# Kernel optimization log

Hardware: AMD Instinct MI355X
Metric: run time of the kernel (lower is better)

Reference implementation:

```python
import jax, jax.numpy as jnp
import numpy as np

DT = 0.001
TAU_SYN_INV = 200.0
TAU_MEM_INV = 100.0
V_TH = 1.0

SEQ_LEN, BATCH, IN_DIM, HIDDEN, OUT_DIM = 1000, 128, 5, 512, 2


def setup_inputs() -> dict:
    key = jax.random.key(0)
    k_x, k_in, k_rec, k_out = jax.random.split(key, 4)
    x = jax.random.normal(k_x, (SEQ_LEN, BATCH, IN_DIM), dtype=jnp.float32)
    # input, recurrent and readout weights (Kaiming-ish scaling)
    w_in = jax.random.normal(k_in, (HIDDEN, IN_DIM), dtype=jnp.float32) / np.sqrt(IN_DIM)
    w_rec = jax.random.normal(k_rec, (HIDDEN, HIDDEN), dtype=jnp.float32) / np.sqrt(HIDDEN)
    w_out = jax.random.normal(k_out, (OUT_DIM, HIDDEN), dtype=jnp.float32) / np.sqrt(HIDDEN)
    return {"x": x, "w_in": w_in, "w_rec": w_rec, "w_out": w_out}


def _snn_forward(x, w_in, w_rec, w_out):
    T, B, _ = x.shape
    H, O = w_rec.shape[0], w_out.shape[0]
    dtype = x.dtype
    beta_syn = 1.0 - DT * TAU_SYN_INV  # synaptic current decay

    def step(carry, x_t):
        z, v, i, vo, io = carry
        # recurrent LIF layer
        i_in = x_t @ w_in.T + z @ w_rec.T            # [B,H]
        v_dec = v + DT * TAU_MEM_INV * (-v + i)      # leaky membrane integration
        z_new = (v_dec > V_TH).astype(dtype)         # spike (heaviside)
        v_new = jnp.where(z_new > 0, 0.0, v_dec)     # reset to v_reset=0
        i_new = i * beta_syn + i_in
        # linear readout (no bias) into LI feedforward cell
        y = z_new @ w_out.T                          # [B,O]
        vo_new = vo + DT * TAU_MEM_INV * (-vo + io)
        io_new = io * beta_syn + y
        return (z_new, v_new, i_new, vo_new, io_new), vo_new

    init = (
        jnp.zeros((B, H), dtype), jnp.zeros((B, H), dtype), jnp.zeros((B, H), dtype),
        jnp.zeros((B, O), dtype), jnp.zeros((B, O), dtype),
    )
    _, voltages = jax.lax.scan(step, init, x)
    return voltages  # [T, B, O] stacked readout voltages


def reference(x, w_in, w_rec, w_out):
    return _snn_forward(x, w_in, w_rec, w_out)
```

## Files before the change

### kernel.cpp

```cpp
#include <hip/hip_runtime.h>

#define HID 512
#define TSTEPS 1000
#define NB 128
#define NIN 5
#define NOUT 2

__global__ void snn_prep(const float* __restrict__ w_rec, float* __restrict__ wT) {
  int idx = blockIdx.x * 256 + threadIdx.x;
  if (idx < (HID + 1) * HID) {
    int j = idx >> 9;
    int h = idx & (HID - 1);
    wT[idx] = (j < HID) ? w_rec[h * HID + j] : 0.0f;
  }
}

__global__ __launch_bounds__(HID) void snn_main(
    const float* __restrict__ x,
    const float* __restrict__ w_in,
    const float* __restrict__ w_out,
    const float* __restrict__ wT,
    float* __restrict__ out)
{
#pragma clang fp contract(off)
  const int b = blockIdx.x;
  const int tid = threadIdx.x;
  const int lane = tid & 63;
  const int wv = tid >> 6;

  __shared__ unsigned long long s_mask[8];
  __shared__ int __align__(16) s_list[HID + 32];
  __shared__ float s_y[16];
  __shared__ float s_x[2][8];

  const float win0 = w_in[tid * NIN + 0];
  const float win1 = w_in[tid * NIN + 1];
  const float win2 = w_in[tid * NIN + 2];
  const float win3 = w_in[tid * NIN + 3];
  const float win4 = w_in[tid * NIN + 4];
  const float wo0 = w_out[tid];
  const float wo1 = w_out[HID + tid];

  float v = 0.0f, cur = 0.0f;
  float vo = 0.0f, io = 0.0f;

  if (tid < NIN) s_x[0][tid] = x[b * NIN + tid];
  __syncthreads();

  int total = 0;

  for (int t = 0; t < TSTEPS; ++t) {
    float racc = 0.0f;
    int n = 0;
    for (; n + 64 < total; n += 32) {
      int idxs[32];
#pragma unroll
      for (int q = 0; q < 8; ++q) {
        int4 jv = *reinterpret_cast<const int4*>(&s_list[n + 4 * q]);
        idxs[4 * q + 0] = jv.x; idxs[4 * q + 1] = jv.y;
        idxs[4 * q + 2] = jv.z; idxs[4 * q + 3] = jv.w;
      }
      float wbuf[32];
#pragma unroll
      for (int k = 0; k < 32; ++k) wbuf[k] = wT[idxs[k] * HID + tid];
#pragma unroll
      for (int k = 0; k < 32; ++k) racc = __fadd_rn(racc, wbuf[k]);
    }
    const bool hasA = (n < total);
    const bool hasB = (n + 32 < total);
    float wbufA[32], wbufB[32];
    if (hasA) {
      int idxs[32];
#pragma unroll
      for (int q = 0; q < 8; ++q) {
        int4 jv = *reinterpret_cast<const int4*>(&s_list[n + 4 * q]);
        idxs[4 * q + 0] = jv.x; idxs[4 * q + 1] = jv.y;
        idxs[4 * q + 2] = jv.z; idxs[4 * q + 3] = jv.w;
      }
#pragma unroll
      for (int k = 0; k < 32; ++k) wbufA[k] = wT[idxs[k] * HID + tid];
    }
    if (hasB) {
      int idxs[32];
#pragma unroll
      for (int q = 0; q < 8; ++q) {
        int4 jv = *reinterpret_cast<const int4*>(&s_list[n + 32 + 4 * q]);
        idxs[4 * q + 0] = jv.x; idxs[4 * q + 1] = jv.y;
        idxs[4 * q + 2] = jv.z; idxs[4 * q + 3] = jv.w;
      }
#pragma unroll
      for (int k = 0; k < 32; ++k) wbufB[k] = wT[idxs[k] * HID + tid];
    }

    const float* sx = s_x[t & 1];
    float a = __fmul_rn(sx[0], win0);
    a = fmaf(sx[1], win1, a);
    a = fmaf(sx[2], win2, a);
    a = fmaf(sx[3], win3, a);
    a = fmaf(sx[4], win4, a);

    const float vd = __fadd_rn(v, __fmul_rn(0.1f, __fsub_rn(cur, v)));
    const bool spike = vd > 1.0f;
    v = spike ? 0.0f : vd;

    float r0 = spike ? wo0 : 0.0f;
    float r1 = spike ? wo1 : 0.0f;
#pragma unroll
    for (int off = 1; off < 64; off <<= 1) {
      r0 = __fadd_rn(r0, __shfl_xor(r0, off, 64));
      r1 = __fadd_rn(r1, __shfl_xor(r1, off, 64));
    }
    const unsigned long long m = __ballot(spike);
    if (lane == 0) { s_mask[wv] = m; s_y[wv] = r0; s_y[8 + wv] = r1; }
    if (t + 1 < TSTEPS && tid < NIN)
      s_x[(t + 1) & 1][tid] = x[(size_t)(t + 1) * NB * NIN + b * NIN + tid];

    if (hasA) {
#pragma unroll
      for (int k = 0; k < 32; ++k) racc = __fadd_rn(racc, wbufA[k]);
    }
    if (hasB) {
#pragma unroll
      for (int k = 0; k < 32; ++k) racc = __fadd_rn(racc, wbufB[k]);
    }
    cur = __fadd_rn(__fmul_rn(0.8f, cur), __fadd_rn(a, racc));

    __syncthreads();

    int base = 0, tot = 0;
#pragma unroll
    for (int w2 = 0; w2 < 8; ++w2) {
      const int c = __popcll(s_mask[w2]);
      base += (w2 < wv) ? c : 0;
      tot += c;
    }
    if (spike) {
      const int pos = base + __popcll(m & ((1ull << lane) - 1ull));
      s_list[pos] = tid;
    }
    const int padded = (tot + 31) & ~31;
    if (tid >= tot && tid < padded) s_list[tid] = HID;

    if (tid < NOUT) {
      float y = 0.0f;
#pragma unroll
      for (int w2 = 0; w2 < 8; ++w2) y = __fadd_rn(y, s_y[tid * 8 + w2]);
      const float von = __fadd_rn(vo, __fmul_rn(0.1f, __fsub_rn(io, vo)));
      io = __fadd_rn(__fmul_rn(0.8f, io), y);
      vo = von;
      out[(size_t)t * NB * NOUT + b * NOUT + tid] = von;
    }

    __syncthreads();
    total = padded;
  }
}

extern "C" void kernel_launch(void* const* d_in, const int* in_sizes, int n_in,
                              void* d_out, int out_size, void* d_ws, size_t ws_size,
                              hipStream_t stream) {
  const float* x     = (const float*)d_in[0];
  const float* w_in  = (const float*)d_in[1];
  const float* w_rec = (const float*)d_in[2];
  const float* w_out = (const float*)d_in[3];
  float* out = (float*)d_out;
  float* wT = (float*)d_ws;

  const int prep_elems = (HID + 1) * HID;
  snn_prep<<<(prep_elems + 255) / 256, 256, 0, stream>>>(w_rec, wT);
  snn_main<<<NB, HID, 0, stream>>>(x, w_in, w_out, wT, out);
}
```

Measured before the change: 1.577 ms.

## Process two neurons per thread and fold readout into sparse spike gather

Each thread now handles two hidden neurons and loads float2 weight pairs from a padded transposed weight matrix. That matrix also carries the readout weights as extra columns, so the readout is computed by the same sparse gather as the recurrent input. Spike lists are built per wave into double-buffered segments with byte offsets and a packed count word, which removes one of the two block barriers per timestep. Output writes are deferred by one step, and x is prefetched into registers. In exchange the block holds fewer threads, each with more serial gather work, and the addressing becomes more complex.

```diff
diff --git a/kernel.cpp b/kernel.cpp
--- a/kernel.cpp
+++ b/kernel.cpp
@@ -5,21 +5,30 @@
 #define NB 128
 #define NIN 5
 #define NOUT 2
+#define ROWW 516
+#define ROWB (ROWW * 4)
+#define DUMMYOFF (HID * ROWB)
 
-__global__ void snn_prep(const float* __restrict__ w_rec, float* __restrict__ wT) {
+__global__ void snn_prep(const float* __restrict__ w_rec,
+                         const float* __restrict__ w_out,
+                         float* __restrict__ wT2) {
   int idx = blockIdx.x * 256 + threadIdx.x;
-  if (idx < (HID + 1) * HID) {
-    int j = idx >> 9;
-    int h = idx & (HID - 1);
-    wT[idx] = (j < HID) ? w_rec[h * HID + j] : 0.0f;
+  const int total = (HID + 1) * ROWW;
+  if (idx >= total) return;
+  int j = idx / ROWW;
+  int h = idx - j * ROWW;
+  float v = 0.0f;
+  if (j < HID) {
+    if (h < HID) v = w_rec[h * HID + j];
+    else if (h < HID + NOUT) v = w_out[(h - HID) * HID + j];
   }
+  wT2[idx] = v;
 }
 
-__global__ __launch_bounds__(HID) void snn_main(
+__global__ __launch_bounds__(320) void snn_main(
     const float* __restrict__ x,
     const float* __restrict__ w_in,
-    const float* __restrict__ w_out,
-    const float* __restrict__ wT,
+    const float* __restrict__ wT2,
     float* __restrict__ out)
 {
 #pragma clang fp contract(off)
@@ -27,132 +36,145 @@
   const int tid = threadIdx.x;
   const int lane = tid & 63;
   const int wv = tid >> 6;
+  const int h0 = tid * 2;
 
-  __shared__ unsigned long long s_mask[8];
-  __shared__ int __align__(16) s_list[HID + 32];
-  __shared__ float s_y[16];
-  __shared__ float s_x[2][8];
+  __shared__ int __align__(16) s_seg[2][4][132];
+  __shared__ unsigned int s_pcnt[2];
 
-  const float win0 = w_in[tid * NIN + 0];
-  const float win1 = w_in[tid * NIN + 1];
-  const float win2 = w_in[tid * NIN + 2];
-  const float win3 = w_in[tid * NIN + 3];
-  const float win4 = w_in[tid * NIN + 4];
-  const float wo0 = w_out[tid];
-  const float wo1 = w_out[HID + tid];
+  float wi00 = 0, wi01 = 0, wi02 = 0, wi03 = 0, wi04 = 0;
+  float wi10 = 0, wi11 = 0, wi12 = 0, wi13 = 0, wi14 = 0;
+  if (tid < 256) {
+    const float* wa = w_in + h0 * NIN;
+    wi00 = wa[0]; wi01 = wa[1]; wi02 = wa[2]; wi03 = wa[3]; wi04 = wa[4];
+    const float* wb = w_in + (h0 + 1) * NIN;
+    wi10 = wb[0]; wi11 = wb[1]; wi12 = wb[2]; wi13 = wb[3]; wi14 = wb[4];
+  }
 
-  float v = 0.0f, cur = 0.0f;
-  float vo = 0.0f, io = 0.0f;
+  float v0 = 0, v1 = 0, c0 = 0, c1 = 0;
+  float io0 = 0, io1 = 0, vo0 = 0, vo1 = 0;
+  float pend0 = 0, pend1 = 0;
 
-  if (tid < NIN) s_x[0][tid] = x[b * NIN + tid];
+  float xr0, xr1, xr2, xr3, xr4;
+  {
+    const float* xp = x + (size_t)b * NIN;
+    xr0 = xp[0]; xr1 = xp[1]; xr2 = xp[2]; xr3 = xp[3]; xr4 = xp[4];
+  }
+
+  if (tid == 0) s_pcnt[0] = 0;
   __syncthreads();
 
-  int total = 0;
+  const char* wtb = (const char*)wT2 + (size_t)h0 * 4;
 
   for (int t = 0; t < TSTEPS; ++t) {
-    float racc = 0.0f;
-    int n = 0;
-    for (; n + 64 < total; n += 32) {
-      int idxs[32];
-#pragma unroll
-      for (int q = 0; q < 8; ++q) {
-        int4 jv = *reinterpret_cast<const int4*>(&s_list[n + 4 * q]);
-        idxs[4 * q + 0] = jv.x; idxs[4 * q + 1] = jv.y;
-        idxs[4 * q + 2] = jv.z; idxs[4 * q + 3] = jv.w;
-      }
-      float wbuf[32];
-#pragma unroll
-      for (int k = 0; k < 32; ++k) wbuf[k] = wT[idxs[k] * HID + tid];
-#pragma unroll
-      for (int k = 0; k < 32; ++k) racc = __fadd_rn(racc, wbuf[k]);
-    }
-    const bool hasA = (n < total);
-    const bool hasB = (n + 32 < total);
-    float wbufA[32], wbufB[32];
-    if (hasA) {
-      int idxs[32];
-#pragma unroll
-      for (int q = 0; q < 8; ++q) {
-        int4 jv = *reinterpret_cast<const int4*>(&s_list[n + 4 * q]);
-        idxs[4 * q + 0] = jv.x; idxs[4 * q + 1] = jv.y;
-        idxs[4 * q + 2] = jv.z; idxs[4 * q + 3] = jv.w;
-      }
-#pragma unroll
-      for (int k = 0; k < 32; ++k) wbufA[k] = wT[idxs[k] * HID + tid];
-    }
-    if (hasB) {
-      int idxs[32];
-#pragma unroll
-      for (int q = 0; q < 8; ++q) {
-        int4 jv = *reinterpret_cast<const int4*>(&s_list[n + 32 + 4 * q]);
-        idxs[4 * q + 0] = jv.x; idxs[4 * q + 1] = jv.y;
-        idxs[4 * q + 2] = jv.z; idxs[4 * q + 3] = jv.w;
-      }
-#pragma unroll
-      for (int k = 0; k < 32; ++k) wbufB[k] = wT[idxs[k] * HID + tid];
+    const int rb = t & 1, wbuf = rb ^ 1;
+
+    if (tid == 256 && t > 0) {
+      float2 po; po.x = pend0; po.y = pend1;
+      *(float2*)(out + (size_t)(t - 1) * NB * NOUT + b * NOUT) = po;
     }
 
-    const float* sx = s_x[t & 1];
-    float a = __fmul_rn(sx[0], win0);
-    a = fmaf(sx[1], win1, a);
-    a = fmaf(sx[2], win2, a);
-    a = fmaf(sx[3], win3, a);
-    a = fmaf(sx[4], win4, a);
-
-    const float vd = __fadd_rn(v, __fmul_rn(0.1f, __fsub_rn(cur, v)));
-    const bool spike = vd > 1.0f;
-    v = spike ? 0.0f : vd;
-
-    float r0 = spike ? wo0 : 0.0f;
-    float r1 = spike ? wo1 : 0.0f;
-#pragma unroll
-    for (int off = 1; off < 64; off <<= 1) {
-      r0 = __fadd_rn(r0, __shfl_xor(r0, off, 64));
-      r1 = __fadd_rn(r1, __shfl_xor(r1, off, 64));
-    }
-    const unsigned long long m = __ballot(spike);
-    if (lane == 0) { s_mask[wv] = m; s_y[wv] = r0; s_y[8 + wv] = r1; }
-    if (t + 1 < TSTEPS && tid < NIN)
-      s_x[(t + 1) & 1][tid] = x[(size_t)(t + 1) * NB * NIN + b * NIN + tid];
-
-    if (hasA) {
-#pragma unroll
-      for (int k = 0; k < 32; ++k) racc = __fadd_rn(racc, wbufA[k]);
-    }
-    if (hasB) {
-#pragma unroll
-      for (int k = 0; k < 32; ++k) racc = __fadd_rn(racc, wbufB[k]);
-    }
-    cur = __fadd_rn(__fmul_rn(0.8f, cur), __fadd_rn(a, racc));
-
-    __syncthreads();
-
-    int base = 0, tot = 0;
-#pragma unroll
-    for (int w2 = 0; w2 < 8; ++w2) {
-      const int c = __popcll(s_mask[w2]);
-      base += (w2 < wv) ? c : 0;
-      tot += c;
-    }
-    if (spike) {
-      const int pos = base + __popcll(m & ((1ull << lane) - 1ull));
-      s_list[pos] = tid;
-    }
-    const int padded = (tot + 31) & ~31;
-    if (tid >= tot && tid < padded) s_list[tid] = HID;
-
-    if (tid < NOUT) {
-      float y = 0.0f;
-#pragma unroll
-      for (int w2 = 0; w2 < 8; ++w2) y = __fadd_rn(y, s_y[tid * 8 + w2]);
-      const float von = __fadd_rn(vo, __fmul_rn(0.1f, __fsub_rn(io, vo)));
-      io = __fadd_rn(__fmul_rn(0.8f, io), y);
-      vo = von;
-      out[(size_t)t * NB * NOUT + b * NOUT + tid] = von;
+    float nx0, nx1, nx2, nx3, nx4;
+    {
+      const int tn = (t + 1 < TSTEPS) ? t + 1 : t;
+      const float* xp = x + ((size_t)tn * NB + b) * NIN;
+      nx0 = xp[0]; nx1 = xp[1]; nx2 = xp[2]; nx3 = xp[3]; nx4 = xp[4];
     }
 
+    const unsigned int pw = s_pcnt[rb];
+    int pc0 = __builtin_amdgcn_readfirstlane((int)(pw & 255u));
+    int pc1 = __builtin_amdgcn_readfirstlane((int)((pw >> 8) & 255u));
+    int pc2 = __builtin_amdgcn_readfirstlane((int)((pw >> 16) & 255u));
+    int pc3 = __builtin_amdgcn_readfirstlane((int)((pw >> 24) & 255u));
+    const int b1 = pc0, b2v = b1 + pc1, b3v = b2v + pc2;
+    const int tot = b3v + pc3;
+    const int ng = tot >> 2;
+
+    float racc0 = 0.0f, racc1 = 0.0f;
+    if (h0 < HID + NOUT) {
+      const char* segbase = (const char*)&s_seg[rb][0][0];
+
+#define SEGADDR(GI, AP) { int w_ = 0, bw_ = 0;                         \
+      if ((GI) >= b1)  { w_ = 1; bw_ = b1;  }                          \
+      if ((GI) >= b2v) { w_ = 2; bw_ = b2v; }                          \
+      if ((GI) >= b3v) { w_ = 3; bw_ = b3v; }                          \
+      AP = segbase + w_ * 528 + ((GI) - bw_) * 4; }
+#define STAGE(JJ, F0, F1, F2, F3, G) { const char* ap_;                \
+      SEGADDR((G) * 4, ap_);                                           \
+      JJ = *(const int4*)ap_;                                          \
+      F0 = *(const float2*)(wtb + JJ.x);                               \
+      F1 = *(const float2*)(wtb + JJ.y);                               \
+      F2 = *(const float2*)(wtb + JJ.z);                               \
+      F3 = *(const float2*)(wtb + JJ.w); }
+#define CONSUME(F0, F1, F2, F3) {                                      \
+      racc0 = __fadd_rn(racc0, F0.x); racc1 = __fadd_rn(racc1, F0.y);  \
+      racc0 = __fadd_rn(racc0, F1.x); racc1 = __fadd_rn(racc1, F1.y);  \
+      racc0 = __fadd_rn(racc0, F2.x); racc1 = __fadd_rn(racc1, F2.y);  \
+      racc0 = __fadd_rn(racc0, F3.x); racc1 = __fadd_rn(racc1, F3.y); }
+
+      if (ng > 0) {
+        int4 jA, jB;
+        float2 a0, a1, a2, a3, q0, q1, q2, q3;
+        STAGE(jA, a0, a1, a2, a3, 0);
+        int g = 1;
+        for (; g + 1 < ng; g += 2) {
+          STAGE(jB, q0, q1, q2, q3, g);
+          CONSUME(a0, a1, a2, a3);
+          STAGE(jA, a0, a1, a2, a3, g + 1);
+          CONSUME(q0, q1, q2, q3);
+        }
+        if (g < ng) {
+          STAGE(jB, q0, q1, q2, q3, g);
+          CONSUME(a0, a1, a2, a3);
+          CONSUME(q0, q1, q2, q3);
+        } else {
+          CONSUME(a0, a1, a2, a3);
+        }
+      }
+    }
+
+    if (tid < 256) {
+      float a0 = __fmul_rn(xr0, wi00);
+      a0 = fmaf(xr1, wi01, a0); a0 = fmaf(xr2, wi02, a0);
+      a0 = fmaf(xr3, wi03, a0); a0 = fmaf(xr4, wi04, a0);
+      float a1 = __fmul_rn(xr0, wi10);
+      a1 = fmaf(xr1, wi11, a1); a1 = fmaf(xr2, wi12, a1);
+      a1 = fmaf(xr3, wi13, a1); a1 = fmaf(xr4, wi14, a1);
+
+      const float vd0 = __fadd_rn(v0, __fmul_rn(0.1f, __fsub_rn(c0, v0)));
+      const float vd1 = __fadd_rn(v1, __fmul_rn(0.1f, __fsub_rn(c1, v1)));
+      const bool s0 = vd0 > 1.0f;
+      const bool s1 = vd1 > 1.0f;
+      v0 = s0 ? 0.0f : vd0;
+      v1 = s1 ? 0.0f : vd1;
+      c0 = __fadd_rn(__fmul_rn(0.8f, c0), __fadd_rn(a0, racc0));
+      c1 = __fadd_rn(__fmul_rn(0.8f, c1), __fadd_rn(a1, racc1));
+
+      const unsigned long long me = __ballot(s0);
+      const unsigned long long mo = __ballot(s1);
+      const unsigned long long below = (1ull << lane) - 1ull;
+      const int cb = __popcll(me & below) + __popcll(mo & below);
+      const int cnt = __popcll(me) + __popcll(mo);
+      const int pcw = (cnt + 3) & ~3;
+      int* seg = &s_seg[wbuf][wv][0];
+      if (s0) seg[cb] = h0 * ROWB;
+      if (s1) seg[cb + (s0 ? 1 : 0)] = (h0 + 1) * ROWB;
+      if (lane < pcw - cnt) seg[cnt + lane] = DUMMYOFF;
+      if (lane == 0) ((unsigned char*)&s_pcnt[wbuf])[wv] = (unsigned char)pcw;
+    } else if (tid == 256) {
+      io0 = __fadd_rn(__fmul_rn(0.8f, io0), racc0);
+      io1 = __fadd_rn(__fmul_rn(0.8f, io1), racc1);
+      vo0 = __fadd_rn(vo0, __fmul_rn(0.1f, __fsub_rn(io0, vo0)));
+      vo1 = __fadd_rn(vo1, __fmul_rn(0.1f, __fsub_rn(io1, vo1)));
+      pend0 = vo0; pend1 = vo1;
+    }
+
+    xr0 = nx0; xr1 = nx1; xr2 = nx2; xr3 = nx3; xr4 = nx4;
     __syncthreads();
-    total = padded;
+  }
+
+  if (tid == 256) {
+    float2 po; po.x = pend0; po.y = pend1;
+    *(float2*)(out + (size_t)(TSTEPS - 1) * NB * NOUT + b * NOUT) = po;
   }
 }
 
@@ -164,9 +186,9 @@
   const float* w_rec = (const float*)d_in[2];
   const float* w_out = (const float*)d_in[3];
   float* out = (float*)d_out;
-  float* wT = (float*)d_ws;
+  float* wT2 = (float*)d_ws;
 
-  const int prep_elems = (HID + 1) * HID;
-  snn_prep<<<(prep_elems + 255) / 256, 256, 0, stream>>>(w_rec, wT);
-  snn_main<<<NB, HID, 0, stream>>>(x, w_in, w_out, wT, out);
+  const int prep_elems = (HID + 1) * ROWW;
+  snn_prep<<<(prep_elems + 255) / 256, 256, 0, stream>>>(w_rec, w_out, wT2);
+  snn_main<<<NB, 320, 0, stream>>>(x, w_in, wT2, out);
 }
```

New measurement: 1.402 ms. -11.1%, faster.
